# Performance work log

Hardware: AMD Instinct MI355X
Metric: run time of the kernel (lower is better)

## Reference

```python
import jax, jax.numpy as jnp
import numpy as np

B, C, H, W = 4, 512, 128, 128
CI = C // 2   # inter_planes
CQ = C // 8   # q/k dim in CrossAttention


def conv1x1(x, w, b=None):
    # x: [B,Cin,H,W], w: [Cout,Cin]
    y = jnp.einsum('oc,bchw->bohw', w, x)
    if b is not None:
        y = y + b[None, :, None, None]
    return y


def setup_inputs() -> dict:
    key = jax.random.key(0)
    ks = jax.random.split(key, 13)
    s = 0.05
    return {
        'x': jax.random.normal(ks[0], (B, C, H, W), jnp.float32),
        # SCCA gating params (1x1 convs, no bias except conv_up)
        'w_q_right': jax.random.normal(ks[1], (1, C), jnp.float32) * s,
        'w_v_right': jax.random.normal(ks[2], (CI, C), jnp.float32) * s,
        'w_up': jax.random.normal(ks[3], (C, CI), jnp.float32) * s,
        'b_up': jnp.zeros((C,), jnp.float32),
        'w_q_left': jax.random.normal(ks[4], (CI, C), jnp.float32) * s,
        'w_v_left': jax.random.normal(ks[5], (CI, C), jnp.float32) * s,
        # CrossAttention params (1x1 convs with bias)
        'wq': jax.random.normal(ks[6], (CQ, C), jnp.float32) * s,
        'bq': jnp.zeros((CQ,), jnp.float32),
        'wk': jax.random.normal(ks[7], (CQ, C), jnp.float32) * s,
        'bk': jnp.zeros((CQ,), jnp.float32),
        'wv': jax.random.normal(ks[8], (C, C), jnp.float32) * s,
        'bv': jnp.zeros((C,), jnp.float32),
        'gamma': jnp.asarray(0.5, jnp.float32),
    }


def cross_attention(x, wq, bq, wk, bk, wv, bv, gamma):
    # criss-cross attention: each pixel attends to its row and column
    b, c, h, w = x.shape
    q = conv1x1(x, wq, bq)   # [B,CQ,H,W]
    k = conv1x1(x, wk, bk)   # [B,CQ,H,W]
    v = conv1x1(x, wv, bv)   # [B,C,H,W]
    # column (H) affinities with -inf on the self diagonal (as in INF())
    diag = jnp.where(jnp.eye(h, dtype=bool), -jnp.inf, 0.0).astype(x.dtype)
    e_h = jnp.einsum('bchw,bcgw->bhwg', q, k) + diag[None, :, None, :]  # [B,H,W,H]
    e_w = jnp.einsum('bchw,bchv->bhwv', q, k)                            # [B,H,W,W]
    att = jax.nn.softmax(jnp.concatenate([e_h, e_w], axis=-1), axis=-1)  # [B,H,W,H+W]
    a_h, a_w = att[..., :h], att[..., h:]
    out_h = jnp.einsum('bcgw,bhwg->bchw', v, a_h)
    out_w = jnp.einsum('bchv,bhwv->bchw', v, a_w)
    return gamma * (out_h + out_w) + x


def spatial_weighted(x, w_q_right, w_v_right, w_up, b_up):
    b, c, h, w = x.shape
    input_x = conv1x1(x, w_v_right).reshape(b, CI, h * w)       # [B,CI,HW]
    mask = jax.nn.softmax(conv1x1(x, w_q_right).reshape(b, h * w), axis=-1)  # [B,HW]
    ctx = jnp.einsum('bcn,bn->bc', input_x, mask)               # [B,CI]
    ctx = jnp.einsum('oc,bc->bo', w_up, ctx) + b_up             # [B,C]
    mask_ch = jax.nn.sigmoid(ctx)[:, :, None, None]
    return x * mask_ch


def channel_weighted(x, w_q_left, w_v_left):
    b, c, h, w = x.shape
    g_x = conv1x1(x, w_q_left)                                  # [B,CI,H,W]
    avg = g_x.mean(axis=(2, 3))                                 # [B,CI]
    theta = conv1x1(x, w_v_left).reshape(b, CI, h * w)          # [B,CI,HW]
    ctx = jax.nn.softmax(jnp.einsum('bc,bcn->bn', avg, theta), axis=-1)
    mask_sp = jax.nn.sigmoid(ctx).reshape(b, 1, h, w)
    return x * mask_sp


def reference(x, w_q_right, w_v_right, w_up, b_up, w_q_left, w_v_left,
              wq, bq, wk, bk, wv, bv, gamma):
    cc = spatial_weighted(x, w_q_right, w_v_right, w_up, b_up)
    cc = cross_attention(cc, wq, bq, wk, bk, wv, bv, gamma)
    cs = channel_weighted(x, w_q_left, w_v_left)
    cs = cross_attention(cs, wq, bq, wk, bk, wv, bv, gamma)
    out = cs + cc
    out = cross_attention(out, wq, bq, wk, bk, wv, bv, gamma)
    return out
```

## Files before the change

### kernel.cpp

```cpp
#include <hip/hip_runtime.h>
#include <hip/hip_bf16.h>
#include <math.h>

typedef __hip_bfloat16 bf16;
typedef __attribute__((ext_vector_type(8))) short s16x8;
typedef __attribute__((ext_vector_type(4))) float f32x4;

constexpr int Bn  = 4;
constexpr int Cn  = 512;
constexpr int Hn  = 128;
constexpr int Wn  = 128;
constexpr int Nn  = Hn * Wn;
constexpr int CQn = 64;
constexpr int CIn = 256;

__device__ __forceinline__ float bf2f(bf16 v){ return __bfloat162float(v); }
__device__ __forceinline__ bf16  f2bf(float v){ return __float2bfloat16(v); }

__device__ __forceinline__ void gload_lds16(const void* g, void* l){
  __builtin_amdgcn_global_load_lds(
      (const __attribute__((address_space(1))) unsigned int*)g,
      (__attribute__((address_space(3))) unsigned int*)l,
      16, 0, 0);
}


__global__ __launch_bounds__(256) void k_dotc(const float* __restrict__ x,
                                              const float* __restrict__ w,
                                              int wstride,
                                              float* __restrict__ out){
  int t = blockIdx.x * 256 + threadIdx.x;
  int b = t >> 14;
  const float* wp = w + (size_t)b * wstride;
  const float* xp = x + (size_t)b * Cn * Nn + (t & (Nn - 1));
  float acc = 0.f;
  #pragma unroll 8
  for (int c = 0; c < Cn; ++c) acc += wp[c] * xp[(size_t)c * Nn];
  out[t] = acc;
}

__global__ __launch_bounds__(256) void k_rowmean(const float* __restrict__ x,
                                                 float* __restrict__ out,
                                                 float scale){
  int bc = blockIdx.x;
  const float* xp = x + (size_t)bc * Nn;
  float acc = 0.f;
  for (int n = threadIdx.x; n < Nn; n += 256) acc += xp[n];
  for (int o = 32; o > 0; o >>= 1) acc += __shfl_down(acc, o);
  __shared__ float red[4];
  if ((threadIdx.x & 63) == 0) red[threadIdx.x >> 6] = acc;
  __syncthreads();
  if (threadIdx.x == 0) out[bc] = (red[0] + red[1] + red[2] + red[3]) * scale;
}

__global__ __launch_bounds__(256) void k_rowdot(const float* __restrict__ W,
                                                const float* __restrict__ vec,
                                                float* __restrict__ out){
  __shared__ float vs[Cn];
  int b = blockIdx.x, t = threadIdx.x;
  for (int j = t; j < Cn; j += 256) vs[j] = vec[b * Cn + j];
  __syncthreads();
  const float4* wp = (const float4*)(W + (size_t)t * Cn);
  float a = 0.f;
  #pragma unroll 4
  for (int j = 0; j < Cn / 4; ++j){
    float4 w4 = wp[j];
    a += w4.x * vs[4*j] + w4.y * vs[4*j+1] + w4.z * vs[4*j+2] + w4.w * vs[4*j+3];
  }
  out[b * CIn + t] = a;
}

__global__ __launch_bounds__(256) void k_coldot(const float* __restrict__ W,
                                                const float* __restrict__ vec,
                                                float* __restrict__ out){
  __shared__ float vs[CIn];
  int b = blockIdx.y, t = threadIdx.x;
  int c = blockIdx.x * 256 + t;
  if (t < CIn) vs[t] = vec[b * CIn + t];
  __syncthreads();
  float a = 0.f;
  #pragma unroll 8
  for (int j = 0; j < CIn; ++j) a += W[(size_t)j * Cn + c] * vs[j];
  out[b * Cn + c] = a;
}

__global__ __launch_bounds__(256) void k_mch2(const float* __restrict__ w_up,
                                              const float* __restrict__ b_up,
                                              const float* __restrict__ ctx,
                                              float* __restrict__ mch){
  __shared__ float cs[CIn];
  int b = blockIdx.y, t = threadIdx.x;
  int o = blockIdx.x * 256 + t;
  if (t < CIn) cs[t] = ctx[b * CIn + t];
  __syncthreads();
  const float4* wp = (const float4*)(w_up + (size_t)o * CIn);
  float a = b_up[o];
  #pragma unroll 4
  for (int j = 0; j < CIn / 4; ++j){
    float4 w4 = wp[j];
    a += w4.x * cs[4*j] + w4.y * cs[4*j+1] + w4.z * cs[4*j+2] + w4.w * cs[4*j+3];
  }
  mch[b * Cn + o] = 1.f / (1.f + expf(-a));
}

__global__ __launch_bounds__(1024) void k_stats(const float* __restrict__ vv,
                                                float* __restrict__ stats){
  int b = blockIdx.x;
  const float* pp = vv + (size_t)b * Nn;
  int t = threadIdx.x;
  float m = -3.4e38f;
  for (int n = t; n < Nn; n += 1024) m = fmaxf(m, pp[n]);
  for (int o = 32; o > 0; o >>= 1) m = fmaxf(m, __shfl_down(m, o));
  __shared__ float red[16];
  int wid = t >> 6, lid = t & 63;
  if (lid == 0) red[wid] = m;
  __syncthreads();
  if (t == 0){
    float q = red[0];
    for (int i = 1; i < 16; i++) q = fmaxf(q, red[i]);
    red[0] = q;
  }
  __syncthreads();
  m = red[0];
  __syncthreads();
  float s = 0.f;
  for (int n = t; n < Nn; n += 1024) s += expf(pp[n] - m);
  for (int o = 32; o > 0; o >>= 1) s += __shfl_down(s, o);
  if (lid == 0) red[wid] = s;
  __syncthreads();
  if (t == 0){
    float q = 0.f;
    for (int i = 0; i < 16; i++) q += red[i];
    stats[b * 2]     = m;
    stats[b * 2 + 1] = q;
  }
}

__global__ __launch_bounds__(256) void k_weighted(const float* __restrict__ x,
                                                  const float* __restrict__ logits,
                                                  const float* __restrict__ stats,
                                                  float* __restrict__ out){
  int bc = blockIdx.x;
  int b = bc >> 9;
  const float* xp = x + (size_t)bc * Nn;
  const float* lp = logits + (size_t)b * Nn;
  float m = stats[b * 2], den = stats[b * 2 + 1];
  float acc = 0.f;
  for (int n = threadIdx.x; n < Nn; n += 256) acc += xp[n] * expf(lp[n] - m);
  for (int o = 32; o > 0; o >>= 1) acc += __shfl_down(acc, o);
  __shared__ float red[4];
  if ((threadIdx.x & 63) == 0) red[threadIdx.x >> 6] = acc;
  __syncthreads();
  if (threadIdx.x == 0) out[bc] = (red[0] + red[1] + red[2] + red[3]) / den;
}

__global__ __launch_bounds__(256) void k_msp(const float* __restrict__ lg,
                                             const float* __restrict__ stats,
                                             float* __restrict__ msp){
  int t = blockIdx.x * 256 + threadIdx.x;
  int b = t >> 14;
  float v = expf(lg[t] - stats[b * 2]) / stats[b * 2 + 1];
  msp[t] = 1.f / (1.f + expf(-v));
}

__global__ __launch_bounds__(256) void k_applyT2(const float* __restrict__ x,
                                                 const float* __restrict__ mch,
                                                 bf16* __restrict__ out_hi,
                                                 bf16* __restrict__ out_lo){
  __shared__ bf16 th_[32][33];
  __shared__ bf16 tl_[32][33];
  int nt = blockIdx.x, ct = blockIdx.y, b = blockIdx.z;
  int n0 = nt * 32, c0 = ct * 32;
  int t = threadIdx.x;
  #pragma unroll
  for (int kk = 0; kk < 4; ++kk){
    int idx = t + kk * 256;
    int cl = idx >> 5, nl = idx & 31;
    float v = x[((size_t)(b * Cn + c0 + cl)) * Nn + n0 + nl] * mch[b * Cn + c0 + cl];
    bf16 h = f2bf(v);
    th_[cl][nl] = h;
    tl_[cl][nl] = f2bf(v - bf2f(h));
  }
  __syncthreads();
  #pragma unroll
  for (int kk = 0; kk < 4; ++kk){
    int idx = t + kk * 256;
    int nl = idx >> 5, cl = idx & 31;
    size_t o = ((size_t)(b * Nn + n0 + nl)) * Cn + c0 + cl;
    out_hi[o] = th_[cl][nl];
    out_lo[o] = tl_[cl][nl];
  }
}

__global__ __launch_bounds__(256) void k_cvt_T2(const float* __restrict__ x,
                                                const float* __restrict__ msp,
                                                bf16* __restrict__ out_hi,
                                                bf16* __restrict__ out_lo){
  __shared__ bf16 th_[32][33];
  __shared__ bf16 tl_[32][33];
  int nt = blockIdx.x, ct = blockIdx.y, b = blockIdx.z;
  int n0 = nt * 32, c0 = ct * 32;
  int t = threadIdx.x;
  #pragma unroll
  for (int kk = 0; kk < 4; ++kk){
    int idx = t + kk * 256;
    int cl = idx >> 5, nl = idx & 31;
    float v = x[((size_t)(b * Cn + c0 + cl)) * Nn + n0 + nl] * msp[b * Nn + n0 + nl];
    bf16 h = f2bf(v);
    th_[cl][nl] = h;
    tl_[cl][nl] = f2bf(v - bf2f(h));
  }
  __syncthreads();
  #pragma unroll
  for (int kk = 0; kk < 4; ++kk){
    int idx = t + kk * 256;
    int nl = idx >> 5, cl = idx & 31;
    size_t o = ((size_t)(b * Nn + n0 + nl)) * Cn + c0 + cl;
    out_hi[o] = th_[cl][nl];
    out_lo[o] = tl_[cl][nl];
  }
}


__global__ __launch_bounds__(256) void k_cvt_w(const float* __restrict__ in,
                                               bf16* __restrict__ out, int n){
  int t = blockIdx.x * 256 + threadIdx.x;
  if (t < n) out[t] = f2bf(in[t]);
}

__global__ __launch_bounds__(256) void k_prep_wqk(const float* __restrict__ wq,
                                                  const float* __restrict__ wk,
                                                  const float* __restrict__ bq,
                                                  const float* __restrict__ bk,
                                                  bf16* __restrict__ wqk_hi,
                                                  bf16* __restrict__ wqk_lo,
                                                  float* __restrict__ bqk){
  int t = blockIdx.x * 256 + threadIdx.x;
  int o = t >> 9, c = t & 511;
  float v = (o < 64) ? wq[(size_t)o * Cn + c] : wk[(size_t)(o - 64) * Cn + c];
  bf16 h = f2bf(v);
  wqk_hi[t] = h;
  wqk_lo[t] = f2bf(v - bf2f(h));
  if (t < 128) bqk[t] = (t < 64) ? bq[t] : bk[t - 64];
}

__global__ __launch_bounds__(256) void k_cvt_T(const float* __restrict__ in,
                                               bf16* __restrict__ out_hi,
                                               bf16* __restrict__ out_lo){
  __shared__ bf16 th_[32][33];
  __shared__ bf16 tl_[32][33];
  int nt = blockIdx.x, ct = blockIdx.y, b = blockIdx.z;
  int n0 = nt * 32, c0 = ct * 32;
  int t = threadIdx.x;
  #pragma unroll
  for (int kk = 0; kk < 4; ++kk){
    int idx = t + kk * 256;
    int cl = idx >> 5, nl = idx & 31;
    float v = in[((size_t)(b * Cn + c0 + cl)) * Nn + n0 + nl];
    bf16 h = f2bf(v);
    th_[cl][nl] = h;
    tl_[cl][nl] = f2bf(v - bf2f(h));
  }
  __syncthreads();
  #pragma unroll
  for (int kk = 0; kk < 4; ++kk){
    int idx = t + kk * 256;
    int nl = idx >> 5, cl = idx & 31;
    size_t o = ((size_t)(b * Nn + n0 + nl)) * Cn + c0 + cl;
    out_hi[o] = th_[cl][nl];
    out_lo[o] = tl_[cl][nl];
  }
}


__global__ __launch_bounds__(256) void k_v_mfma(const bf16* __restrict__ xT,
                                                const bf16* __restrict__ wvb,
                                                const float* __restrict__ bv,
                                                bf16* __restrict__ v){
  __shared__ short As[128 * 64];
  __shared__ short Bs[128 * 64];
  __shared__ float bvs[128];
  int lin = blockIdx.x;
  int swz = (lin & 7) * 256 + (lin >> 3);
  int cb = (swz & 3) * 128;
  int nb = ((swz >> 2) & 127) * 128;
  int b  = swz >> 9;
  int t = threadIdx.x, lane = t & 63, wid = t >> 6;
  int wm = wid >> 1, wn = wid & 1;
  int l15 = lane & 15, l4 = lane >> 4;
  if (t < 128) bvs[t] = bv[cb + t];
  f32x4 acc[4][4];
  #pragma unroll
  for (int i = 0; i < 4; i++)
    #pragma unroll
    for (int j = 0; j < 4; j++) acc[i][j] = (f32x4){0.f, 0.f, 0.f, 0.f};

  const bf16* wp = wvb + (size_t)cb * Cn;
  const bf16* xp = xT + ((size_t)b * Nn + nb) * Cn;
  int r8 = lane >> 3;
  int kc = (lane & 7) * 8;
  for (int kt = 0; kt < 8; ++kt){
    int k0 = kt * 64;
    #pragma unroll
    for (int j = 0; j < 4; ++j){
      int inst = wid * 4 + j;
      int row = inst * 8 + r8;
      gload_lds16(wp + (size_t)row * Cn + k0 + kc, (char*)As + inst * 1024);
      gload_lds16(xp + (size_t)row * Cn + k0 + kc, (char*)Bs + inst * 1024);
    }
    __syncthreads();
    #pragma unroll
    for (int kk = 0; kk < 64; kk += 32){
      s16x8 a[4], bb[4];
      #pragma unroll
      for (int mi = 0; mi < 4; mi++)
        a[mi] = *(const s16x8*)&As[(wm * 64 + mi * 16 + l15) * 64 + kk + l4 * 8];
      #pragma unroll
      for (int ni = 0; ni < 4; ni++)
        bb[ni] = *(const s16x8*)&Bs[(wn * 64 + ni * 16 + l15) * 64 + kk + l4 * 8];
      #pragma unroll
      for (int mi = 0; mi < 4; mi++)
        #pragma unroll
        for (int ni = 0; ni < 4; ni++)
          acc[mi][ni] = __builtin_amdgcn_mfma_f32_16x16x32_bf16(a[mi], bb[ni], acc[mi][ni], 0, 0, 0);
    }
    __syncthreads();
  }
  #pragma unroll
  for (int mi = 0; mi < 4; mi++){
    #pragma unroll
    for (int r = 0; r < 4; r++){
      int cl = wm * 64 + mi * 16 + l4 * 4 + r;
      int c  = cb + cl;
      float bias = bvs[cl];
      #pragma unroll
      for (int ni = 0; ni < 4; ni++){
        int n = nb + wn * 64 + ni * 16 + l15;
        v[((size_t)(b * Cn + c)) * Nn + n] = f2bf(acc[mi][ni][r] + bias);
      }
    }
  }
}

__global__ __launch_bounds__(256) void k_qk_mfma(const bf16* __restrict__ xT_hi,
                                                 const bf16* __restrict__ xT_lo,
                                                 const bf16* __restrict__ wqk_hi,
                                                 const bf16* __restrict__ wqk_lo,
                                                 const float* __restrict__ bqk,
                                                 bf16* __restrict__ q,
                                                 bf16* __restrict__ k){
  __shared__ short Ah[128 * 64];
  __shared__ short Al[128 * 64];
  __shared__ short Bh[128 * 64];
  __shared__ short Bl[128 * 64];
  __shared__ float bs[128];
  int nb = blockIdx.x * 128, b = blockIdx.y;
  int t = threadIdx.x, lane = t & 63, wid = t >> 6;
  int wm = wid >> 1, wn = wid & 1;
  int l15 = lane & 15, l4 = lane >> 4;
  if (t < 128) bs[t] = bqk[t];
  f32x4 acc[4][4];
  #pragma unroll
  for (int i = 0; i < 4; i++)
    #pragma unroll
    for (int j = 0; j < 4; j++) acc[i][j] = (f32x4){0.f, 0.f, 0.f, 0.f};

  const bf16* xh = xT_hi + ((size_t)b * Nn + nb) * Cn;
  const bf16* xl = xT_lo + ((size_t)b * Nn + nb) * Cn;
  int r8 = lane >> 3;
  int kc = (lane & 7) * 8;
  for (int kt = 0; kt < 8; ++kt){
    int k0 = kt * 64;
    #pragma unroll
    for (int j = 0; j < 4; ++j){
      int inst = wid * 4 + j;
      int row = inst * 8 + r8;
      size_t off = (size_t)row * Cn + k0 + kc;
      gload_lds16(wqk_hi + off, (char*)Ah + inst * 1024);
      gload_lds16(wqk_lo + off, (char*)Al + inst * 1024);
      gload_lds16(xh + off,     (char*)Bh + inst * 1024);
      gload_lds16(xl + off,     (char*)Bl + inst * 1024);
    }
    __syncthreads();
    #pragma unroll
    for (int kk = 0; kk < 64; kk += 32){
      s16x8 ah[4], al[4], bh[4], bl[4];
      #pragma unroll
      for (int mi = 0; mi < 4; mi++){
        int idx = (wm * 64 + mi * 16 + l15) * 64 + kk + l4 * 8;
        ah[mi] = *(const s16x8*)&Ah[idx];
        al[mi] = *(const s16x8*)&Al[idx];
      }
      #pragma unroll
      for (int ni = 0; ni < 4; ni++){
        int idx = (wn * 64 + ni * 16 + l15) * 64 + kk + l4 * 8;
        bh[ni] = *(const s16x8*)&Bh[idx];
        bl[ni] = *(const s16x8*)&Bl[idx];
      }
      #pragma unroll
      for (int mi = 0; mi < 4; mi++)
        #pragma unroll
        for (int ni = 0; ni < 4; ni++){
          acc[mi][ni] = __builtin_amdgcn_mfma_f32_16x16x32_bf16(ah[mi], bh[ni], acc[mi][ni], 0, 0, 0);
          acc[mi][ni] = __builtin_amdgcn_mfma_f32_16x16x32_bf16(ah[mi], bl[ni], acc[mi][ni], 0, 0, 0);
          acc[mi][ni] = __builtin_amdgcn_mfma_f32_16x16x32_bf16(al[mi], bh[ni], acc[mi][ni], 0, 0, 0);
        }
    }
    __syncthreads();
  }
  #pragma unroll
  for (int mi = 0; mi < 4; mi++){
    #pragma unroll
    for (int r = 0; r < 4; r++){
      int o = wm * 64 + mi * 16 + l4 * 4 + r;
      float bias = bs[o];
      #pragma unroll
      for (int ni = 0; ni < 4; ni++){
        int n = nb + wn * 64 + ni * 16 + l15;
        float val = acc[mi][ni][r] + bias;
        if (o < 64) q[((size_t)(b * CQn + o)) * Nn + n]        = f2bf(val);
        else        k[((size_t)(b * CQn + o - 64)) * Nn + n]   = f2bf(val);
      }
    }
  }
}


__global__ __launch_bounds__(256) void k_att_h(const bf16* __restrict__ qT,
                                               const bf16* __restrict__ kT,
                                               const bf16* __restrict__ vT,
                                               float* __restrict__ mh,
                                               float* __restrict__ sh,
                                               bf16* __restrict__ ohX){
  __shared__ float smem[16384];
  float* qs = smem;
  float* ks = smem + 8192;
  char* attb = (char*)smem;
  char* vbb  = (char*)smem + 32768;
  int w = blockIdx.x, b = blockIdx.y;
  int t = threadIdx.x, lane = t & 63, wid = t >> 6;
  const bf16* qp = qT + (size_t)(b * Wn + w) * CQn * Hn;
  const bf16* kp = kT + (size_t)(b * Wn + w) * CQn * Hn;
  for (int i = t; i < 8192; i += 256){ qs[i] = bf2f(qp[i]); ks[i] = bf2f(kp[i]); }
  __syncthreads();
  int hg = t >> 3, gg = t & 7;
  float acc[4][16];
  #pragma unroll
  for (int i = 0; i < 4; i++)
    #pragma unroll
    for (int j = 0; j < 16; j++) acc[i][j] = 0.f;
  for (int c = 0; c < CQn; ++c){
    float qv[4], kv[16];
    #pragma unroll
    for (int i = 0; i < 4; i++) qv[i] = qs[c * 128 + hg * 4 + i];
    #pragma unroll
    for (int j = 0; j < 16; j++) kv[j] = ks[c * 128 + gg + 8 * j];
    #pragma unroll
    for (int i = 0; i < 4; i++)
      #pragma unroll
      for (int j = 0; j < 16; j++) acc[i][j] += qv[i] * kv[j];
  }
  float mrow[4], srow[4];
  #pragma unroll
  for (int i = 0; i < 4; i++){
    int hrow = hg * 4 + i;
    #pragma unroll
    for (int j = 0; j < 16; j++)
      if (hrow == gg + 8 * j) acc[i][j] = -1e30f;
    float m = acc[i][0];
    #pragma unroll
    for (int j = 1; j < 16; j++) m = fmaxf(m, acc[i][j]);
    m = fmaxf(m, __shfl_xor(m, 1));
    m = fmaxf(m, __shfl_xor(m, 2));
    m = fmaxf(m, __shfl_xor(m, 4));
    mrow[i] = m;
    float s = 0.f;
    #pragma unroll
    for (int j = 0; j < 16; j++){ acc[i][j] = expf(acc[i][j] - m); s += acc[i][j]; }
    s += __shfl_xor(s, 1);
    s += __shfl_xor(s, 2);
    s += __shfl_xor(s, 4);
    srow[i] = s;
  }
  __syncthreads();
  #pragma unroll
  for (int i = 0; i < 4; i++)
    #pragma unroll
    for (int j = 0; j < 16; j++){
      int h = hg * 4 + i, g = gg + 8 * j;
      bf16 bv = f2bf(acc[i][j]);
      int byte = (h * 256 + g * 2) ^ ((h & 7) << 4);
      *(unsigned short*)(attb + byte) = *(unsigned short*)&bv;
    }
  if (gg == 0){
    #pragma unroll
    for (int i = 0; i < 4; i++){
      mh[(size_t)(b * Wn + w) * Hn + hg * 4 + i] = mrow[i];
      sh[(size_t)(b * Wn + w) * Hn + hg * 4 + i] = srow[i];
    }
  }
  __syncthreads();
  int wm = wid >> 1, wn = wid & 1;
  int l15 = lane & 15, l4 = lane >> 4;
  for (int cb = 0; cb < Cn; cb += 128){
    const bf16* vp = vT + ((size_t)(b * Wn + w) * Cn + cb) * Hn;
    for (int s = t; s < 2048; s += 256){
      int row = s >> 4, seg = s & 15;
      s16x8 d = *(const s16x8*)(vp + (size_t)row * Hn + seg * 8);
      int byte = (row * 256 + seg * 16) ^ ((row & 7) << 4);
      *(s16x8*)(vbb + byte) = d;
    }
    __syncthreads();
    f32x4 acc2[4][4];
    #pragma unroll
    for (int i = 0; i < 4; i++)
      #pragma unroll
      for (int j = 0; j < 4; j++) acc2[i][j] = (f32x4){0.f, 0.f, 0.f, 0.f};
    #pragma unroll
    for (int kk = 0; kk < 128; kk += 32){
      s16x8 a[4], bb[4];
      #pragma unroll
      for (int mi = 0; mi < 4; mi++){
        int row = wm * 64 + mi * 16 + l15;
        int byte = (row * 256 + (kk + l4 * 8) * 2) ^ ((row & 7) << 4);
        a[mi] = *(const s16x8*)(vbb + byte);
      }
      #pragma unroll
      for (int ni = 0; ni < 4; ni++){
        int row = wn * 64 + ni * 16 + l15;
        int byte = (row * 256 + (kk + l4 * 8) * 2) ^ ((row & 7) << 4);
        bb[ni] = *(const s16x8*)(attb + byte);
      }
      #pragma unroll
      for (int mi = 0; mi < 4; mi++)
        #pragma unroll
        for (int ni = 0; ni < 4; ni++)
          acc2[mi][ni] = __builtin_amdgcn_mfma_f32_16x16x32_bf16(a[mi], bb[ni], acc2[mi][ni], 0, 0, 0);
    }
    bf16* op = ohX + ((size_t)(b * Cn + cb)) * Nn + (size_t)w * Hn;
    #pragma unroll
    for (int mi = 0; mi < 4; mi++)
      #pragma unroll
      for (int r = 0; r < 4; r++){
        int cl = wm * 64 + mi * 16 + l4 * 4 + r;
        #pragma unroll
        for (int ni = 0; ni < 4; ni++){
          int h = wn * 64 + ni * 16 + l15;
          op[(size_t)cl * Nn + h] = f2bf(acc2[mi][ni][r]);
        }
      }
    __syncthreads();
  }
}

__global__ __launch_bounds__(256) void k_att_w(const bf16* __restrict__ q,
                                               const bf16* __restrict__ k,
                                               const bf16* __restrict__ v,
                                               float* __restrict__ mw,
                                               float* __restrict__ sw,
                                               bf16* __restrict__ ow){
  __shared__ float smem[16384];
  float* qs = smem;
  float* ks = smem + 8192;
  char* attb = (char*)smem;
  char* vbb  = (char*)smem + 32768;
  int h = blockIdx.x, b = blockIdx.y;
  int t = threadIdx.x, lane = t & 63, wid = t >> 6;
  for (int i = t; i < 8192; i += 256){
    int c = i >> 7, wl = i & 127;
    size_t base = ((size_t)(b * CQn + c) * Hn + h) * Wn + wl;
    qs[i] = bf2f(q[base]);
    ks[i] = bf2f(k[base]);
  }
  __syncthreads();
  int wg = t >> 3, vg = t & 7;
  float acc[4][16];
  #pragma unroll
  for (int i = 0; i < 4; i++)
    #pragma unroll
    for (int j = 0; j < 16; j++) acc[i][j] = 0.f;
  for (int c = 0; c < CQn; ++c){
    float qv[4], kv[16];
    #pragma unroll
    for (int i = 0; i < 4; i++) qv[i] = qs[c * 128 + wg * 4 + i];
    #pragma unroll
    for (int j = 0; j < 16; j++) kv[j] = ks[c * 128 + vg + 8 * j];
    #pragma unroll
    for (int i = 0; i < 4; i++)
      #pragma unroll
      for (int j = 0; j < 16; j++) acc[i][j] += qv[i] * kv[j];
  }
  float mrow[4], srow[4];
  #pragma unroll
  for (int i = 0; i < 4; i++){
    float m = acc[i][0];
    #pragma unroll
    for (int j = 1; j < 16; j++) m = fmaxf(m, acc[i][j]);
    m = fmaxf(m, __shfl_xor(m, 1));
    m = fmaxf(m, __shfl_xor(m, 2));
    m = fmaxf(m, __shfl_xor(m, 4));
    mrow[i] = m;
    float s = 0.f;
    #pragma unroll
    for (int j = 0; j < 16; j++){ acc[i][j] = expf(acc[i][j] - m); s += acc[i][j]; }
    s += __shfl_xor(s, 1);
    s += __shfl_xor(s, 2);
    s += __shfl_xor(s, 4);
    srow[i] = s;
  }
  __syncthreads();
  #pragma unroll
  for (int i = 0; i < 4; i++)
    #pragma unroll
    for (int j = 0; j < 16; j++){
      int wr = wg * 4 + i, g = vg + 8 * j;
      bf16 bv = f2bf(acc[i][j]);
      int byte = (wr * 256 + g * 2) ^ ((wr & 7) << 4);
      *(unsigned short*)(attb + byte) = *(unsigned short*)&bv;
    }
  if (vg == 0){
    #pragma unroll
    for (int i = 0; i < 4; i++){
      mw[(size_t)(b * Hn + h) * Wn + wg * 4 + i] = mrow[i];
      sw[(size_t)(b * Hn + h) * Wn + wg * 4 + i] = srow[i];
    }
  }
  __syncthreads();
  int wm = wid >> 1, wn = wid & 1;
  int l15 = lane & 15, l4 = lane >> 4;
  for (int cb = 0; cb < Cn; cb += 128){
    const bf16* vp = v + (size_t)(b * Cn + cb) * Nn + (size_t)h * Wn;
    for (int s = t; s < 2048; s += 256){
      int row = s >> 4, seg = s & 15;
      s16x8 d = *(const s16x8*)(vp + (size_t)row * Nn + seg * 8);
      int byte = (row * 256 + seg * 16) ^ ((row & 7) << 4);
      *(s16x8*)(vbb + byte) = d;
    }
    __syncthreads();
    f32x4 acc2[4][4];
    #pragma unroll
    for (int i = 0; i < 4; i++)
      #pragma unroll
      for (int j = 0; j < 4; j++) acc2[i][j] = (f32x4){0.f, 0.f, 0.f, 0.f};
    #pragma unroll
    for (int kk = 0; kk < 128; kk += 32){
      s16x8 a[4], bb[4];
      #pragma unroll
      for (int mi = 0; mi < 4; mi++){
        int row = wm * 64 + mi * 16 + l15;
        int byte = (row * 256 + (kk + l4 * 8) * 2) ^ ((row & 7) << 4);
        a[mi] = *(const s16x8*)(vbb + byte);
      }
      #pragma unroll
      for (int ni = 0; ni < 4; ni++){
        int row = wn * 64 + ni * 16 + l15;
        int byte = (row * 256 + (kk + l4 * 8) * 2) ^ ((row & 7) << 4);
        bb[ni] = *(const s16x8*)(attb + byte);
      }
      #pragma unroll
      for (int mi = 0; mi < 4; mi++)
        #pragma unroll
        for (int ni = 0; ni < 4; ni++)
          acc2[mi][ni] = __builtin_amdgcn_mfma_f32_16x16x32_bf16(a[mi], bb[ni], acc2[mi][ni], 0, 0, 0);
    }
    bf16* op = ow + (size_t)(b * Cn + cb) * Nn + (size_t)h * Wn;
    #pragma unroll
    for (int mi = 0; mi < 4; mi++)
      #pragma unroll
      for (int r = 0; r < 4; r++){
        int cl = wm * 64 + mi * 16 + l4 * 4 + r;
        #pragma unroll
        for (int ni = 0; ni < 4; ni++){
          int wr = wn * 64 + ni * 16 + l15;
          op[(size_t)cl * Nn + wr] = f2bf(acc2[mi][ni][r]);
        }
      }
    __syncthreads();
  }
}

__global__ __launch_bounds__(256) void k_alpha(const float* __restrict__ mh,
                                               const float* __restrict__ sh,
                                               const float* __restrict__ mw,
                                               const float* __restrict__ sw,
                                               float* __restrict__ ahT,
                                               float* __restrict__ aw){
  int t = blockIdx.x * 256 + threadIdx.x;
  int b = t >> 14;
  int hw = t & (Nn - 1);
  int h = hw >> 7, w = hw & 127;
  size_t ih = (size_t)(b * Wn + w) * Hn + h;
  size_t iw = t;
  float mhv = mh[ih], mwv = mw[iw];
  float M = fmaxf(mhv, mwv);
  float eh_ = expf(mhv - M), ew_ = expf(mwv - M);
  float inv = 1.f / (sh[ih] * eh_ + sw[iw] * ew_);
  ahT[t] = eh_ * inv;
  aw[t]  = ew_ * inv;
}


__global__ __launch_bounds__(256) void k_trans(const bf16* __restrict__ in,
                                               bf16* __restrict__ out,
                                               int CH){
  __shared__ bf16 tile[32][33];
  int tl = blockIdx.x, c = blockIdx.y, b = blockIdx.z;
  int th = tl >> 2, tw = tl & 3;
  int h0 = th * 32, w0 = tw * 32;
  int t = threadIdx.x;
  const bf16* ip = in + ((size_t)(b * CH + c)) * Nn;
  #pragma unroll
  for (int kk = 0; kk < 4; ++kk){
    int idx = t + kk * 256;
    int hl = idx >> 5, wl = idx & 31;
    tile[hl][wl] = ip[(h0 + hl) * Wn + w0 + wl];
  }
  __syncthreads();
  #pragma unroll
  for (int kk = 0; kk < 4; ++kk){
    int idx = t + kk * 256;
    int wl = idx >> 5, hl = idx & 31;
    out[((size_t)(b * Wn + w0 + wl) * CH + c) * Hn + h0 + hl] = tile[hl][wl];
  }
}

__global__ __launch_bounds__(256) void k_fuse2(const float* __restrict__ in,
                                               const float* __restrict__ maskc,
                                               const float* __restrict__ maskn,
                                               const bf16* __restrict__ ohX,
                                               const bf16* __restrict__ ow,
                                               const float* __restrict__ ahT,
                                               const float* __restrict__ aw,
                                               const float* __restrict__ addend,
                                               const float* __restrict__ gamma,
                                               float* __restrict__ out){
  __shared__ unsigned short tileT[128][138];
  int c = blockIdx.x, b = blockIdx.y;
  int t = threadIdx.x;
  float g = gamma[0];
  float mc = maskc ? maskc[b * Cn + c] : 1.f;
  const bf16* ohp = ohX + ((size_t)(b * Cn + c)) * Nn;
  #pragma unroll
  for (int i = 0; i < 8; ++i){
    int s = t + i * 256;
    int w = s >> 4, seg = s & 15;
    s16x8 d = *(const s16x8*)(ohp + (size_t)s * 8);
    #pragma unroll
    for (int j = 0; j < 8; ++j)
      tileT[seg * 8 + j][w] = (unsigned short)d[j];
  }
  __syncthreads();
  size_t base = ((size_t)(b * Cn + c)) * Nn;
  #pragma unroll
  for (int i = 0; i < 16; ++i){
    int o = t + i * 256;
    int h = o >> 5, w4 = (o & 31) * 4;
    size_t idx = base + (size_t)h * Wn + w4;
    size_t aidx = (size_t)b * Nn + (size_t)h * Wn + w4;
    float4 inv = *(const float4*)(in + idx);
    ushort4 owv = *(const ushort4*)((const unsigned short*)ow + idx);
    float4 ah4 = *(const float4*)(ahT + aidx);
    float4 aw4 = *(const float4*)(aw + aidx);
    float4 mn4 = maskn ? *(const float4*)(maskn + aidx) : (float4){1.f,1.f,1.f,1.f};
    float r[4];
    #pragma unroll
    for (int j = 0; j < 4; ++j){
      unsigned short uh = tileT[h][w4 + j];
      unsigned short uo = ((const unsigned short*)&owv)[j];
      float ohv = bf2f(*(bf16*)&uh);
      float owf = bf2f(*(bf16*)&uo);
      float iv  = ((const float*)&inv)[j] * mc * ((const float*)&mn4)[j];
      float ahv = ((const float*)&ah4)[j];
      float awv = ((const float*)&aw4)[j];
      r[j] = g * (ahv * ohv + awv * owf) + iv;
    }
    if (addend){
      float4 av = *(const float4*)(addend + idx);
      r[0] += av.x; r[1] += av.y; r[2] += av.z; r[3] += av.w;
    }
    float4 o4 = { r[0], r[1], r[2], r[3] };
    *(float4*)(out + idx) = o4;
  }
}


static void run_ca(const float* resid, const float* maskc, const float* maskn,
                   const bf16* wqk_hi, const bf16* wqk_lo,
                   const float* bqk, const bf16* wvb, const float* bv,
                   const float* gamma, const float* addend, float* out,
                   bf16* q, bf16* k, bf16* qT, bf16* kT, bf16* v, bf16* vT,
                   float* mh, float* sh, float* mw, float* sw, float* ahT, float* aw,
                   bf16* xT_hi, bf16* xT_lo, bf16* tmp, hipStream_t stream){
  bf16* ohX = tmp;
  bf16* ow  = tmp + (size_t)Bn * Cn * Nn;
  k_qk_mfma<<<dim3(Nn / 128, Bn), 256, 0, stream>>>(xT_hi, xT_lo, wqk_hi, wqk_lo, bqk, q, k);
  k_trans<<<dim3(16, CQn, Bn), 256, 0, stream>>>(q, qT, CQn);
  k_trans<<<dim3(16, CQn, Bn), 256, 0, stream>>>(k, kT, CQn);
  k_v_mfma<<<2048, 256, 0, stream>>>(xT_hi, wvb, bv, v);
  k_trans<<<dim3(16, Cn, Bn), 256, 0, stream>>>(v, vT, Cn);
  k_att_h<<<dim3(Wn, Bn), 256, 0, stream>>>(qT, kT, vT, mh, sh, ohX);
  k_att_w<<<dim3(Hn, Bn), 256, 0, stream>>>(q, k, v, mw, sw, ow);
  k_alpha<<<Bn * Nn / 256, 256, 0, stream>>>(mh, sh, mw, sw, ahT, aw);
  k_fuse2<<<dim3(Cn, Bn), 256, 0, stream>>>(resid, maskc, maskn, ohX, ow, ahT, aw,
                                            addend, gamma, out);
}

extern "C" void kernel_launch(void* const* d_in, const int* in_sizes, int n_in,
                              void* d_out, int out_size, void* d_ws, size_t ws_size,
                              hipStream_t stream){
  (void)in_sizes; (void)n_in; (void)out_size; (void)ws_size;
  const float* x         = (const float*)d_in[0];
  const float* w_q_right = (const float*)d_in[1];
  const float* w_v_right = (const float*)d_in[2];
  const float* w_up      = (const float*)d_in[3];
  const float* b_up      = (const float*)d_in[4];
  const float* w_q_left  = (const float*)d_in[5];
  const float* w_v_left  = (const float*)d_in[6];
  const float* wq        = (const float*)d_in[7];
  const float* bq        = (const float*)d_in[8];
  const float* wk        = (const float*)d_in[9];
  const float* bk        = (const float*)d_in[10];
  const float* wv        = (const float*)d_in[11];
  const float* bv        = (const float*)d_in[12];
  const float* gamma     = (const float*)d_in[13];

  const size_t SZ_MAP = (size_t)Bn * Cn * Nn;
  char* p = (char*)d_ws;
  float* buf0   = (float*)p; p += SZ_MAP * 4;
  float* buf1   = (float*)p; p += SZ_MAP * 4;
  bf16*  vbuf   = (bf16*)p;  p += SZ_MAP * 2;
  bf16*  vT     = (bf16*)p;  p += SZ_MAP * 2;
  bf16*  qbuf   = (bf16*)p;  p += (size_t)Bn * CQn * Nn * 2;
  bf16*  kbuf   = (bf16*)p;  p += (size_t)Bn * CQn * Nn * 2;
  bf16*  qT     = (bf16*)p;  p += (size_t)Bn * CQn * Nn * 2;
  bf16*  kT     = (bf16*)p;  p += (size_t)Bn * CQn * Nn * 2;
  float* ebuf   = (float*)p; p += (size_t)SZ_MAP * 2;
  float* logits = (float*)p; p += (size_t)Bn * Nn * 4;
  float* ctxlog = (float*)p; p += (size_t)Bn * Nn * 4;
  float* msp    = (float*)p; p += (size_t)Bn * Nn * 4;
  float* xbar   = (float*)p; p += Bn * Cn * 4;
  float* wgt    = (float*)p; p += Bn * Cn * 4;
  float* u      = (float*)p; p += Bn * Cn * 4;
  float* mch    = (float*)p; p += Bn * Cn * 4;
  float* avg    = (float*)p; p += Bn * CIn * 4;
  float* ctx    = (float*)p; p += Bn * CIn * 4;
  float* stats_sp = (float*)p; p += 64;
  float* stats_ch = (float*)p; p += 64;
  bf16*  wvb    = (bf16*)p;  p += (size_t)Cn * Cn * 2;
  bf16*  wqk_hi = (bf16*)p;  p += (size_t)128 * Cn * 2;
  bf16*  wqk_lo = (bf16*)p;  p += (size_t)128 * Cn * 2;
  float* bqk    = (float*)p; p += 128 * 4;
  float* mh     = (float*)p; p += (size_t)Bn * Nn * 4;
  float* sh     = (float*)p; p += (size_t)Bn * Nn * 4;
  float* mw     = (float*)p; p += (size_t)Bn * Nn * 4;
  float* sw     = (float*)p; p += (size_t)Bn * Nn * 4;
  float* ahT    = (float*)p; p += (size_t)Bn * Nn * 4;
  float* aw     = (float*)p; p += (size_t)Bn * Nn * 4;

  bf16*  xT_hi  = (bf16*)ebuf;
  bf16*  xT_lo  = (bf16*)d_out;

  k_cvt_w<<<(Cn * Cn + 255) / 256, 256, 0, stream>>>(wv, wvb, Cn * Cn);
  k_prep_wqk<<<(128 * Cn) / 256, 256, 0, stream>>>(wq, wk, bq, bk, wqk_hi, wqk_lo, bqk);

  k_dotc<<<Bn * Nn / 256, 256, 0, stream>>>(x, w_q_right, 0, logits);
  k_rowmean<<<Bn * Cn, 256, 0, stream>>>(x, xbar, 1.f / Nn);
  k_rowdot<<<Bn, 256, 0, stream>>>(w_q_left, xbar, avg);
  k_coldot<<<dim3(Cn / 256, Bn), 256, 0, stream>>>(w_v_left, avg, u);
  k_stats<<<Bn, 1024, 0, stream>>>(logits, stats_sp);
  k_weighted<<<Bn * Cn, 256, 0, stream>>>(x, logits, stats_sp, wgt);
  k_rowdot<<<Bn, 256, 0, stream>>>(w_v_right, wgt, ctx);
  k_mch2<<<dim3(Cn / 256, Bn), 256, 0, stream>>>(w_up, b_up, ctx, mch);
  k_dotc<<<Bn * Nn / 256, 256, 0, stream>>>(x, u, Cn, ctxlog);
  k_stats<<<Bn, 1024, 0, stream>>>(ctxlog, stats_ch);
  k_msp<<<Bn * Nn / 256, 256, 0, stream>>>(ctxlog, stats_ch, msp);

  k_applyT2<<<dim3(Nn / 32, Cn / 32, Bn), 256, 0, stream>>>(x, mch, xT_hi, xT_lo);
  run_ca(x, mch, nullptr, wqk_hi, wqk_lo, bqk, wvb, bv, gamma, nullptr, buf0,
         qbuf, kbuf, qT, kT, vbuf, vT, mh, sh, mw, sw, ahT, aw,
         xT_hi, xT_lo, (bf16*)d_out, stream);
  k_cvt_T2<<<dim3(Nn / 32, Cn / 32, Bn), 256, 0, stream>>>(x, msp, xT_hi, xT_lo);
  run_ca(x, nullptr, msp, wqk_hi, wqk_lo, bqk, wvb, bv, gamma, buf0, buf0,
         qbuf, kbuf, qT, kT, vbuf, vT, mh, sh, mw, sw, ahT, aw,
         xT_hi, xT_lo, (bf16*)d_out, stream);
  k_cvt_T<<<dim3(Nn / 32, Cn / 32, Bn), 256, 0, stream>>>(buf0, xT_hi, xT_lo);
  run_ca(buf0, nullptr, nullptr, wqk_hi, wqk_lo, bqk, wvb, bv, gamma, nullptr,
         (float*)d_out,
         qbuf, kbuf, qT, kT, vbuf, vT, mh, sh, mw, sw, ahT, aw,
         xT_hi, xT_lo, (bf16*)buf1, stream);
}
```

Measured before the change: 1.400 ms.

## Compute criss-cross attention energies with MFMA using channel-innermost Q/K layout

Replaces the scalar FP32 outer-product computation of row and column attention energies with bf16 MFMA 16x16x32 tiles. A new transpose kernel puts Q and K into a [B,W,H,C] layout so that MFMA operand fragments load directly from global memory. Softmax max and sum reductions now combine across waves through shared memory. The change removes the FP32 LDS staging and FMA loop, at the cost of extra cross-wave reductions and strided global loads in the W-direction kernel.

```diff
diff --git a/kernel.cpp b/kernel.cpp
--- a/kernel.cpp
+++ b/kernel.cpp
@@ -269,6 +269,26 @@
     size_t o = ((size_t)(b * Nn + n0 + nl)) * Cn + c0 + cl;
     out_hi[o] = th_[cl][nl];
     out_lo[o] = tl_[cl][nl];
+  }
+}
+
+__global__ __launch_bounds__(256) void k_trans4(const bf16* __restrict__ in,
+                                                bf16* __restrict__ out){
+  __shared__ bf16 tile[64][33];
+  int wt = blockIdx.x, h = blockIdx.y, b = blockIdx.z;
+  int w0 = wt * 32, t = threadIdx.x;
+  #pragma unroll
+  for (int i = 0; i < 8; ++i){
+    int s = t + i * 256;
+    int c = s >> 5, wl = s & 31;
+    tile[c][wl] = in[((size_t)(b * CQn + c) * Hn + h) * Wn + w0 + wl];
+  }
+  __syncthreads();
+  #pragma unroll
+  for (int i = 0; i < 8; ++i){
+    int s = t + i * 256;
+    int wl = s >> 6, c = s & 63;
+    out[(((size_t)b * Wn + w0 + wl) * Hn + h) * CQn + c] = tile[c][wl];
   }
 }
 
@@ -426,82 +446,118 @@
 }
 
 
-__global__ __launch_bounds__(256) void k_att_h(const bf16* __restrict__ qT,
-                                               const bf16* __restrict__ kT,
+__global__ __launch_bounds__(256) void k_att_h(const bf16* __restrict__ qhw,
+                                               const bf16* __restrict__ khw,
                                                const bf16* __restrict__ vT,
                                                float* __restrict__ mh,
                                                float* __restrict__ sh,
                                                bf16* __restrict__ ohX){
-  __shared__ float smem[16384];
-  float* qs = smem;
-  float* ks = smem + 8192;
-  char* attb = (char*)smem;
-  char* vbb  = (char*)smem + 32768;
+  __shared__ char smem[65536];
+  char* attb = smem;
+  char* vbb  = smem + 32768;
+  float* redm = (float*)(smem + 32768);
+  float* reds = redm + 256;
   int w = blockIdx.x, b = blockIdx.y;
   int t = threadIdx.x, lane = t & 63, wid = t >> 6;
-  const bf16* qp = qT + (size_t)(b * Wn + w) * CQn * Hn;
-  const bf16* kp = kT + (size_t)(b * Wn + w) * CQn * Hn;
-  for (int i = t; i < 8192; i += 256){ qs[i] = bf2f(qp[i]); ks[i] = bf2f(kp[i]); }
-  __syncthreads();
-  int hg = t >> 3, gg = t & 7;
-  float acc[4][16];
-  #pragma unroll
-  for (int i = 0; i < 4; i++)
-    #pragma unroll
-    for (int j = 0; j < 16; j++) acc[i][j] = 0.f;
-  for (int c = 0; c < CQn; ++c){
-    float qv[4], kv[16];
-    #pragma unroll
-    for (int i = 0; i < 4; i++) qv[i] = qs[c * 128 + hg * 4 + i];
-    #pragma unroll
-    for (int j = 0; j < 16; j++) kv[j] = ks[c * 128 + gg + 8 * j];
-    #pragma unroll
-    for (int i = 0; i < 4; i++)
-      #pragma unroll
-      for (int j = 0; j < 16; j++) acc[i][j] += qv[i] * kv[j];
-  }
-  float mrow[4], srow[4];
-  #pragma unroll
-  for (int i = 0; i < 4; i++){
-    int hrow = hg * 4 + i;
-    #pragma unroll
-    for (int j = 0; j < 16; j++)
-      if (hrow == gg + 8 * j) acc[i][j] = -1e30f;
-    float m = acc[i][0];
-    #pragma unroll
-    for (int j = 1; j < 16; j++) m = fmaxf(m, acc[i][j]);
-    m = fmaxf(m, __shfl_xor(m, 1));
-    m = fmaxf(m, __shfl_xor(m, 2));
-    m = fmaxf(m, __shfl_xor(m, 4));
-    mrow[i] = m;
-    float s = 0.f;
-    #pragma unroll
-    for (int j = 0; j < 16; j++){ acc[i][j] = expf(acc[i][j] - m); s += acc[i][j]; }
-    s += __shfl_xor(s, 1);
-    s += __shfl_xor(s, 2);
-    s += __shfl_xor(s, 4);
-    srow[i] = s;
-  }
-  __syncthreads();
-  #pragma unroll
-  for (int i = 0; i < 4; i++)
-    #pragma unroll
-    for (int j = 0; j < 16; j++){
-      int h = hg * 4 + i, g = gg + 8 * j;
-      bf16 bv = f2bf(acc[i][j]);
-      int byte = (h * 256 + g * 2) ^ ((h & 7) << 4);
-      *(unsigned short*)(attb + byte) = *(unsigned short*)&bv;
-    }
-  if (gg == 0){
-    #pragma unroll
-    for (int i = 0; i < 4; i++){
-      mh[(size_t)(b * Wn + w) * Hn + hg * 4 + i] = mrow[i];
-      sh[(size_t)(b * Wn + w) * Hn + hg * 4 + i] = srow[i];
-    }
-  }
-  __syncthreads();
   int wm = wid >> 1, wn = wid & 1;
   int l15 = lane & 15, l4 = lane >> 4;
+
+  const bf16* qp = qhw + ((size_t)(b * Wn + w)) * (Hn * CQn);
+  const bf16* kp = khw + ((size_t)(b * Wn + w)) * (Hn * CQn);
+  f32x4 acc[4][4];
+  #pragma unroll
+  for (int i = 0; i < 4; i++)
+    #pragma unroll
+    for (int j = 0; j < 4; j++) acc[i][j] = (f32x4){0.f, 0.f, 0.f, 0.f};
+  #pragma unroll
+  for (int kk = 0; kk < 64; kk += 32){
+    s16x8 a[4], bb[4];
+    #pragma unroll
+    for (int mi = 0; mi < 4; mi++)
+      a[mi] = *(const s16x8*)(qp + (size_t)(wm * 64 + mi * 16 + l15) * CQn + kk + l4 * 8);
+    #pragma unroll
+    for (int ni = 0; ni < 4; ni++)
+      bb[ni] = *(const s16x8*)(kp + (size_t)(wn * 64 + ni * 16 + l15) * CQn + kk + l4 * 8);
+    #pragma unroll
+    for (int mi = 0; mi < 4; mi++)
+      #pragma unroll
+      for (int ni = 0; ni < 4; ni++)
+        acc[mi][ni] = __builtin_amdgcn_mfma_f32_16x16x32_bf16(a[mi], bb[ni], acc[mi][ni], 0, 0, 0);
+  }
+  if (wm == wn){
+    #pragma unroll
+    for (int mi = 0; mi < 4; mi++)
+      #pragma unroll
+      for (int r = 0; r < 4; r++)
+        if (l15 == l4 * 4 + r) acc[mi][mi][r] = -1e30f;
+  }
+  float rm[4][4];
+  #pragma unroll
+  for (int mi = 0; mi < 4; mi++)
+    #pragma unroll
+    for (int r = 0; r < 4; r++){
+      float m = fmaxf(fmaxf(acc[mi][0][r], acc[mi][1][r]),
+                      fmaxf(acc[mi][2][r], acc[mi][3][r]));
+      m = fmaxf(m, __shfl_xor(m, 1));
+      m = fmaxf(m, __shfl_xor(m, 2));
+      m = fmaxf(m, __shfl_xor(m, 4));
+      m = fmaxf(m, __shfl_xor(m, 8));
+      rm[mi][r] = m;
+    }
+  if (l15 == 0){
+    #pragma unroll
+    for (int mi = 0; mi < 4; mi++)
+      #pragma unroll
+      for (int r = 0; r < 4; r++)
+        redm[wn * 128 + wm * 64 + mi * 16 + l4 * 4 + r] = rm[mi][r];
+  }
+  __syncthreads();
+  float rs[4][4];
+  #pragma unroll
+  for (int mi = 0; mi < 4; mi++)
+    #pragma unroll
+    for (int r = 0; r < 4; r++){
+      int h = wm * 64 + mi * 16 + l4 * 4 + r;
+      float m = fmaxf(redm[h], redm[128 + h]);
+      rm[mi][r] = m;
+      float s = 0.f;
+      #pragma unroll
+      for (int ni = 0; ni < 4; ni++){
+        acc[mi][ni][r] = expf(acc[mi][ni][r] - m);
+        s += acc[mi][ni][r];
+      }
+      s += __shfl_xor(s, 1);
+      s += __shfl_xor(s, 2);
+      s += __shfl_xor(s, 4);
+      s += __shfl_xor(s, 8);
+      rs[mi][r] = s;
+    }
+  if (l15 == 0){
+    #pragma unroll
+    for (int mi = 0; mi < 4; mi++)
+      #pragma unroll
+      for (int r = 0; r < 4; r++)
+        reds[wn * 128 + wm * 64 + mi * 16 + l4 * 4 + r] = rs[mi][r];
+  }
+  __syncthreads();
+  #pragma unroll
+  for (int mi = 0; mi < 4; mi++)
+    #pragma unroll
+    for (int r = 0; r < 4; r++){
+      int h = wm * 64 + mi * 16 + l4 * 4 + r;
+      if (wn == 0 && l15 == 0){
+        mh[(size_t)(b * Wn + w) * Hn + h] = rm[mi][r];
+        sh[(size_t)(b * Wn + w) * Hn + h] = reds[h] + reds[128 + h];
+      }
+      #pragma unroll
+      for (int ni = 0; ni < 4; ni++){
+        int g = wn * 64 + ni * 16 + l15;
+        bf16 bv = f2bf(acc[mi][ni][r]);
+        int byte = (h * 256 + g * 2) ^ ((h & 7) << 4);
+        *(unsigned short*)(attb + byte) = *(unsigned short*)&bv;
+      }
+    }
+  __syncthreads();
   for (int cb = 0; cb < Cn; cb += 128){
     const bf16* vp = vT + ((size_t)(b * Wn + w) * Cn + cb) * Hn;
     for (int s = t; s < 2048; s += 256){
@@ -553,81 +609,111 @@
   }
 }
 
-__global__ __launch_bounds__(256) void k_att_w(const bf16* __restrict__ q,
-                                               const bf16* __restrict__ k,
+__global__ __launch_bounds__(256) void k_att_w(const bf16* __restrict__ qhw,
+                                               const bf16* __restrict__ khw,
                                                const bf16* __restrict__ v,
                                                float* __restrict__ mw,
                                                float* __restrict__ sw,
                                                bf16* __restrict__ ow){
-  __shared__ float smem[16384];
-  float* qs = smem;
-  float* ks = smem + 8192;
-  char* attb = (char*)smem;
-  char* vbb  = (char*)smem + 32768;
+  __shared__ char smem[65536];
+  char* attb = smem;
+  char* vbb  = smem + 32768;
+  float* redm = (float*)(smem + 32768);
+  float* reds = redm + 256;
   int h = blockIdx.x, b = blockIdx.y;
   int t = threadIdx.x, lane = t & 63, wid = t >> 6;
-  for (int i = t; i < 8192; i += 256){
-    int c = i >> 7, wl = i & 127;
-    size_t base = ((size_t)(b * CQn + c) * Hn + h) * Wn + wl;
-    qs[i] = bf2f(q[base]);
-    ks[i] = bf2f(k[base]);
-  }
-  __syncthreads();
-  int wg = t >> 3, vg = t & 7;
-  float acc[4][16];
-  #pragma unroll
-  for (int i = 0; i < 4; i++)
-    #pragma unroll
-    for (int j = 0; j < 16; j++) acc[i][j] = 0.f;
-  for (int c = 0; c < CQn; ++c){
-    float qv[4], kv[16];
-    #pragma unroll
-    for (int i = 0; i < 4; i++) qv[i] = qs[c * 128 + wg * 4 + i];
-    #pragma unroll
-    for (int j = 0; j < 16; j++) kv[j] = ks[c * 128 + vg + 8 * j];
-    #pragma unroll
-    for (int i = 0; i < 4; i++)
-      #pragma unroll
-      for (int j = 0; j < 16; j++) acc[i][j] += qv[i] * kv[j];
-  }
-  float mrow[4], srow[4];
-  #pragma unroll
-  for (int i = 0; i < 4; i++){
-    float m = acc[i][0];
-    #pragma unroll
-    for (int j = 1; j < 16; j++) m = fmaxf(m, acc[i][j]);
-    m = fmaxf(m, __shfl_xor(m, 1));
-    m = fmaxf(m, __shfl_xor(m, 2));
-    m = fmaxf(m, __shfl_xor(m, 4));
-    mrow[i] = m;
-    float s = 0.f;
-    #pragma unroll
-    for (int j = 0; j < 16; j++){ acc[i][j] = expf(acc[i][j] - m); s += acc[i][j]; }
-    s += __shfl_xor(s, 1);
-    s += __shfl_xor(s, 2);
-    s += __shfl_xor(s, 4);
-    srow[i] = s;
-  }
-  __syncthreads();
-  #pragma unroll
-  for (int i = 0; i < 4; i++)
-    #pragma unroll
-    for (int j = 0; j < 16; j++){
-      int wr = wg * 4 + i, g = vg + 8 * j;
-      bf16 bv = f2bf(acc[i][j]);
-      int byte = (wr * 256 + g * 2) ^ ((wr & 7) << 4);
-      *(unsigned short*)(attb + byte) = *(unsigned short*)&bv;
-    }
-  if (vg == 0){
-    #pragma unroll
-    for (int i = 0; i < 4; i++){
-      mw[(size_t)(b * Hn + h) * Wn + wg * 4 + i] = mrow[i];
-      sw[(size_t)(b * Hn + h) * Wn + wg * 4 + i] = srow[i];
-    }
-  }
-  __syncthreads();
   int wm = wid >> 1, wn = wid & 1;
   int l15 = lane & 15, l4 = lane >> 4;
+
+  const bf16* qp = qhw + (size_t)b * Wn * Hn * CQn + (size_t)h * CQn;
+  const bf16* kp = khw + (size_t)b * Wn * Hn * CQn + (size_t)h * CQn;
+  f32x4 acc[4][4];
+  #pragma unroll
+  for (int i = 0; i < 4; i++)
+    #pragma unroll
+    for (int j = 0; j < 4; j++) acc[i][j] = (f32x4){0.f, 0.f, 0.f, 0.f};
+  #pragma unroll
+  for (int kk = 0; kk < 64; kk += 32){
+    s16x8 a[4], bb[4];
+    #pragma unroll
+    for (int mi = 0; mi < 4; mi++)
+      a[mi] = *(const s16x8*)(qp + (size_t)(wm * 64 + mi * 16 + l15) * (Hn * CQn) + kk + l4 * 8);
+    #pragma unroll
+    for (int ni = 0; ni < 4; ni++)
+      bb[ni] = *(const s16x8*)(kp + (size_t)(wn * 64 + ni * 16 + l15) * (Hn * CQn) + kk + l4 * 8);
+    #pragma unroll
+    for (int mi = 0; mi < 4; mi++)
+      #pragma unroll
+      for (int ni = 0; ni < 4; ni++)
+        acc[mi][ni] = __builtin_amdgcn_mfma_f32_16x16x32_bf16(a[mi], bb[ni], acc[mi][ni], 0, 0, 0);
+  }
+  float rm[4][4];
+  #pragma unroll
+  for (int mi = 0; mi < 4; mi++)
+    #pragma unroll
+    for (int r = 0; r < 4; r++){
+      float m = fmaxf(fmaxf(acc[mi][0][r], acc[mi][1][r]),
+                      fmaxf(acc[mi][2][r], acc[mi][3][r]));
+      m = fmaxf(m, __shfl_xor(m, 1));
+      m = fmaxf(m, __shfl_xor(m, 2));
+      m = fmaxf(m, __shfl_xor(m, 4));
+      m = fmaxf(m, __shfl_xor(m, 8));
+      rm[mi][r] = m;
+    }
+  if (l15 == 0){
+    #pragma unroll
+    for (int mi = 0; mi < 4; mi++)
+      #pragma unroll
+      for (int r = 0; r < 4; r++)
+        redm[wn * 128 + wm * 64 + mi * 16 + l4 * 4 + r] = rm[mi][r];
+  }
+  __syncthreads();
+  float rs[4][4];
+  #pragma unroll
+  for (int mi = 0; mi < 4; mi++)
+    #pragma unroll
+    for (int r = 0; r < 4; r++){
+      int wr = wm * 64 + mi * 16 + l4 * 4 + r;
+      float m = fmaxf(redm[wr], redm[128 + wr]);
+      rm[mi][r] = m;
+      float s = 0.f;
+      #pragma unroll
+      for (int ni = 0; ni < 4; ni++){
+        acc[mi][ni][r] = expf(acc[mi][ni][r] - m);
+        s += acc[mi][ni][r];
+      }
+      s += __shfl_xor(s, 1);
+      s += __shfl_xor(s, 2);
+      s += __shfl_xor(s, 4);
+      s += __shfl_xor(s, 8);
+      rs[mi][r] = s;
+    }
+  if (l15 == 0){
+    #pragma unroll
+    for (int mi = 0; mi < 4; mi++)
+      #pragma unroll
+      for (int r = 0; r < 4; r++)
+        reds[wn * 128 + wm * 64 + mi * 16 + l4 * 4 + r] = rs[mi][r];
+  }
+  __syncthreads();
+  #pragma unroll
+  for (int mi = 0; mi < 4; mi++)
+    #pragma unroll
+    for (int r = 0; r < 4; r++){
+      int wr = wm * 64 + mi * 16 + l4 * 4 + r;
+      if (wn == 0 && l15 == 0){
+        mw[(size_t)(b * Hn + h) * Wn + wr] = rm[mi][r];
+        sw[(size_t)(b * Hn + h) * Wn + wr] = reds[wr] + reds[128 + wr];
+      }
+      #pragma unroll
+      for (int ni = 0; ni < 4; ni++){
+        int g = wn * 64 + ni * 16 + l15;
+        bf16 bv = f2bf(acc[mi][ni][r]);
+        int byte = (wr * 256 + g * 2) ^ ((wr & 7) << 4);
+        *(unsigned short*)(attb + byte) = *(unsigned short*)&bv;
+      }
+    }
+  __syncthreads();
   for (int cb = 0; cb < Cn; cb += 128){
     const bf16* vp = v + (size_t)(b * Cn + cb) * Nn + (size_t)h * Wn;
     for (int s = t; s < 2048; s += 256){
@@ -788,18 +874,18 @@
                    const bf16* wqk_hi, const bf16* wqk_lo,
                    const float* bqk, const bf16* wvb, const float* bv,
                    const float* gamma, const float* addend, float* out,
-                   bf16* q, bf16* k, bf16* qT, bf16* kT, bf16* v, bf16* vT,
+                   bf16* q, bf16* k, bf16* qhw, bf16* khw, bf16* v, bf16* vT,
                    float* mh, float* sh, float* mw, float* sw, float* ahT, float* aw,
                    bf16* xT_hi, bf16* xT_lo, bf16* tmp, hipStream_t stream){
   bf16* ohX = tmp;
   bf16* ow  = tmp + (size_t)Bn * Cn * Nn;
   k_qk_mfma<<<dim3(Nn / 128, Bn), 256, 0, stream>>>(xT_hi, xT_lo, wqk_hi, wqk_lo, bqk, q, k);
-  k_trans<<<dim3(16, CQn, Bn), 256, 0, stream>>>(q, qT, CQn);
-  k_trans<<<dim3(16, CQn, Bn), 256, 0, stream>>>(k, kT, CQn);
+  k_trans4<<<dim3(Wn / 32, Hn, Bn), 256, 0, stream>>>(q, qhw);
+  k_trans4<<<dim3(Wn / 32, Hn, Bn), 256, 0, stream>>>(k, khw);
   k_v_mfma<<<2048, 256, 0, stream>>>(xT_hi, wvb, bv, v);
   k_trans<<<dim3(16, Cn, Bn), 256, 0, stream>>>(v, vT, Cn);
-  k_att_h<<<dim3(Wn, Bn), 256, 0, stream>>>(qT, kT, vT, mh, sh, ohX);
-  k_att_w<<<dim3(Hn, Bn), 256, 0, stream>>>(q, k, v, mw, sw, ow);
+  k_att_h<<<dim3(Wn, Bn), 256, 0, stream>>>(qhw, khw, vT, mh, sh, ohX);
+  k_att_w<<<dim3(Hn, Bn), 256, 0, stream>>>(qhw, khw, v, mw, sw, ow);
   k_alpha<<<Bn * Nn / 256, 256, 0, stream>>>(mh, sh, mw, sw, ahT, aw);
   k_fuse2<<<dim3(Cn, Bn), 256, 0, stream>>>(resid, maskc, maskn, ohX, ow, ahT, aw,
                                             addend, gamma, out);
@@ -832,8 +918,8 @@
   bf16*  vT     = (bf16*)p;  p += SZ_MAP * 2;
   bf16*  qbuf   = (bf16*)p;  p += (size_t)Bn * CQn * Nn * 2;
   bf16*  kbuf   = (bf16*)p;  p += (size_t)Bn * CQn * Nn * 2;
-  bf16*  qT     = (bf16*)p;  p += (size_t)Bn * CQn * Nn * 2;
-  bf16*  kT     = (bf16*)p;  p += (size_t)Bn * CQn * Nn * 2;
+  bf16*  qhw    = (bf16*)p;  p += (size_t)Bn * CQn * Nn * 2;
+  bf16*  khw    = (bf16*)p;  p += (size_t)Bn * CQn * Nn * 2;
   float* ebuf   = (float*)p; p += (size_t)SZ_MAP * 2;
   float* logits = (float*)p; p += (size_t)Bn * Nn * 4;
   float* ctxlog = (float*)p; p += (size_t)Bn * Nn * 4;
@@ -877,15 +963,15 @@
 
   k_applyT2<<<dim3(Nn / 32, Cn / 32, Bn), 256, 0, stream>>>(x, mch, xT_hi, xT_lo);
   run_ca(x, mch, nullptr, wqk_hi, wqk_lo, bqk, wvb, bv, gamma, nullptr, buf0,
-         qbuf, kbuf, qT, kT, vbuf, vT, mh, sh, mw, sw, ahT, aw,
+         qbuf, kbuf, qhw, khw, vbuf, vT, mh, sh, mw, sw, ahT, aw,
          xT_hi, xT_lo, (bf16*)d_out, stream);
   k_cvt_T2<<<dim3(Nn / 32, Cn / 32, Bn), 256, 0, stream>>>(x, msp, xT_hi, xT_lo);
   run_ca(x, nullptr, msp, wqk_hi, wqk_lo, bqk, wvb, bv, gamma, buf0, buf0,
-         qbuf, kbuf, qT, kT, vbuf, vT, mh, sh, mw, sw, ahT, aw,
+         qbuf, kbuf, qhw, khw, vbuf, vT, mh, sh, mw, sw, ahT, aw,
          xT_hi, xT_lo, (bf16*)d_out, stream);
   k_cvt_T<<<dim3(Nn / 32, Cn / 32, Bn), 256, 0, stream>>>(buf0, xT_hi, xT_lo);
   run_ca(buf0, nullptr, nullptr, wqk_hi, wqk_lo, bqk, wvb, bv, gamma, nullptr,
          (float*)d_out,
-         qbuf, kbuf, qT, kT, vbuf, vT, mh, sh, mw, sw, ahT, aw,
+         qbuf, kbuf, qhw, khw, vbuf, vT, mh, sh, mw, sw, ahT, aw,
          xT_hi, xT_lo, (bf16*)buf1, stream);
 }
```

After: 1.387 ms. Within noise of the previous version (-0.9%).
